# Optimization experiments

Measured on AMD Instinct MI355X. Metric: run time of the kernel, lower is better.

The kernel has to match this reference:

```python
import jax, jax.numpy as jnp
import numpy as np

INPUT_DIM, HIDDEN, LATENT, HEADS = 4, 32, 2, 4
N_NODES, N_EDGES = 50000, 800000
EPS_BN = 1e-5
NEG_SLOPE = 0.2


def _glorot(key, shape):
    fan_in, fan_out = shape[0], shape[-1]
    lim = jnp.sqrt(6.0 / (fan_in + fan_out))
    return jax.random.uniform(key, shape, jnp.float32, -lim, lim)


def setup_inputs() -> dict:
    key = jax.random.key(0)
    ks = jax.random.split(key, 20)
    x = jax.random.normal(ks[0], (N_NODES, INPUT_DIM), jnp.float32)
    edge_index = jax.random.randint(ks[1], (2, N_EDGES), 0, N_NODES, jnp.int64)

    def gat_params(k, in_ch, out_ch, heads, concat):
        k1, k2, k3 = jax.random.split(k, 3)
        W = _glorot(k1, (in_ch, heads * out_ch))
        a_src = _glorot(k2, (heads, out_ch))
        a_dst = _glorot(k3, (heads, out_ch))
        b = jnp.zeros((heads * out_ch,) if concat else (out_ch,), jnp.float32)
        return W, a_src, a_dst, b

    w_e1, as_e1, ad_e1, b_e1 = gat_params(ks[2], INPUT_DIM, HIDDEN, HEADS, True)
    w_e3, as_e3, ad_e3, b_e3 = gat_params(ks[3], HIDDEN * HEADS, LATENT, 1, False)
    w_d1, as_d1, ad_d1, b_d1 = gat_params(ks[4], LATENT, HIDDEN, HEADS, True)
    w_d3, as_d3, ad_d3, b_d3 = gat_params(ks[5], HIDDEN * HEADS, INPUT_DIM, 1, False)

    return dict(
        x=x, edge_index=edge_index,
        bn_gamma=jnp.ones((INPUT_DIM,), jnp.float32),
        bn_beta=jnp.zeros((INPUT_DIM,), jnp.float32),
        w_e1=w_e1, as_e1=as_e1, ad_e1=ad_e1, b_e1=b_e1,
        w_e3=w_e3, as_e3=as_e3, ad_e3=ad_e3, b_e3=b_e3,
        w_d1=w_d1, as_d1=as_d1, ad_d1=ad_d1, b_d1=b_d1,
        w_d3=w_d3, as_d3=as_d3, ad_d3=ad_d3, b_d3=b_d3,
    )


def gat_conv(x, src, dst, W, a_src, a_dst, b, heads, out_ch, concat):
    """PyG-style GATConv: gather -> attention -> segment softmax -> scatter."""
    n = x.shape[0]
    h = (x @ W).reshape(n, heads, out_ch)                 # [N,H,C]
    alpha_s = jnp.sum(h * a_src, axis=-1)                 # [N,H]
    alpha_d = jnp.sum(h * a_dst, axis=-1)                 # [N,H]
    e = jax.nn.leaky_relu(alpha_s[src] + alpha_d[dst], NEG_SLOPE)  # [E,H]
    # numerically-stable softmax over incoming edges of each dst node
    m = jax.ops.segment_max(e, dst, num_segments=n)
    e = jnp.exp(e - m[dst])
    s = jax.ops.segment_sum(e, dst, num_segments=n)
    a = e / (s[dst] + 1e-16)                              # [E,H]
    msg = h[src] * a[:, :, None]                          # [E,H,C]
    out = jax.ops.segment_sum(msg, dst, num_segments=n)   # [N,H,C]
    out = out.reshape(n, heads * out_ch) if concat else out.mean(axis=1)
    return out + b


def reference(x, edge_index, bn_gamma, bn_beta,
              w_e1, as_e1, ad_e1, b_e1,
              w_e3, as_e3, ad_e3, b_e3,
              w_d1, as_d1, ad_d1, b_d1,
              w_d3, as_d3, ad_d3, b_d3):
    n = x.shape[0]
    # GATConv default add_self_loops=True
    loops = jnp.arange(n, dtype=edge_index.dtype)
    src = jnp.concatenate([edge_index[0], loops])
    dst = jnp.concatenate([edge_index[1], loops])

    # BatchNorm1d (training-mode batch statistics, biased variance)
    mu = x.mean(axis=0)
    var = x.var(axis=0)
    x_in = (x - mu) * jax.lax.rsqrt(var + EPS_BN) * bn_gamma + bn_beta

    enc1 = jax.nn.relu(gat_conv(x_in, src, dst, w_e1, as_e1, ad_e1, b_e1, HEADS, HIDDEN, True))
    latent = gat_conv(enc1, src, dst, w_e3, as_e3, ad_e3, b_e3, 1, LATENT, False)
    dec1 = jax.nn.relu(gat_conv(latent, src, dst, w_d1, as_d1, ad_d1, b_d1, HEADS, HIDDEN, True))
    x_out = gat_conv(dec1, src, dst, w_d3, as_d3, ad_d3, b_d3, 1, INPUT_DIM, False)
    return x_out
```

## Files before the change

kernel.cpp:

```cpp
#include <hip/hip_runtime.h>

#define NN 50000
#define E0 800000
#define ET 850000
#define EPS_BN 1e-5f
#define SLOPE 0.2f
#define NBP 32
#define EPC 4096
#define NCH 208
#define PBITS 7
#define PSZ 128
#define NP 391
#define CAP 3072

__device__ __forceinline__ float lrelu(float v){ return v > 0.f ? v : SLOPE*v; }

__global__ __launch_bounds__(512) void k1_stage(const int* __restrict__ ei, const float* __restrict__ x,
                                                unsigned* __restrict__ pedge, int* __restrict__ gcur,
                                                float* __restrict__ part){
  __shared__ unsigned epk[EPC];
  __shared__ int cc[NP];
  __shared__ int cbase[NP];
  __shared__ float bnlds[8][8];
  const int b=blockIdx.x, t=threadIdx.x;
  for (int i=t;i<NP;i+=512) cc[i]=0;
  __syncthreads();
  int base=b*EPC;
  int nb=min(EPC, ET-base);
  for (int k=t;k<nb;k+=512){
    int e=base+k;
    int src,dst;
    if (e<E0){ src=ei[e]; dst=ei[E0+e]; } else { src=dst=e-E0; }
    epk[k]=((unsigned)src<<16)|(unsigned)dst;
    atomicAdd(&cc[dst>>PBITS],1);
  }
  __syncthreads();
  for (int i=t;i<NP;i+=512){
    int c=cc[i];
    cbase[i] = (c>0) ? atomicAdd(&gcur[i], c) : 0;
  }
  __syncthreads();
  for (int i=t;i<NP;i+=512) cc[i]=0;
  __syncthreads();
  for (int k=t;k<nb;k+=512){
    unsigned w=epk[k];
    int p=(int)((w&0xFFFFu)>>PBITS);
    int lo=atomicAdd(&cc[p],1);
    pedge[p*CAP + cbase[p] + lo]=w;
  }

  if (b<NBP){
    float s[4]={0,0,0,0}, q[4]={0,0,0,0};
    for (int n=b*512+t; n<NN; n+=NBP*512){
      float4 v = reinterpret_cast<const float4*>(x)[n];
      s[0]+=v.x; s[1]+=v.y; s[2]+=v.z; s[3]+=v.w;
      q[0]+=v.x*v.x; q[1]+=v.y*v.y; q[2]+=v.z*v.z; q[3]+=v.w*v.w;
    }
    #pragma unroll
    for (int m=1;m<64;m<<=1){
      #pragma unroll
      for (int i=0;i<4;i++){ s[i]+=__shfl_xor(s[i],m); q[i]+=__shfl_xor(q[i],m); }
    }
    int wid=t>>6, lane=t&63;
    if (lane==0){
      #pragma unroll
      for (int i=0;i<4;i++){ bnlds[wid][i]=s[i]; bnlds[wid][4+i]=q[i]; }
    }
    __syncthreads();
    if (t<8){
      float p=0.f;
      #pragma unroll
      for (int w=0;w<8;w++) p += bnlds[w][t];
      part[b*8+t]=p;
    }
  }
}

__global__ __launch_bounds__(512) void k2_fine(
    const unsigned* __restrict__ pedge, const int* __restrict__ gcur,
    int* __restrict__ rbeg, int* __restrict__ rend, unsigned short* __restrict__ ssrc,
    const float* __restrict__ part, const float* __restrict__ gamma, const float* __restrict__ beta,
    const float* __restrict__ w_e1, const float* __restrict__ as_e1, const float* __restrict__ ad_e1,
    const float* __restrict__ w_d1, const float* __restrict__ as_d1, const float* __restrict__ ad_d1,
    float* __restrict__ sclsft, float* __restrict__ fold){
  const int p=blockIdx.x, t=threadIdx.x;
  int cnt=gcur[p];
  int wbase=p*CAP;
  __shared__ int hist[PSZ], curx[PSZ];
  if (t<PSZ) hist[t]=0;
  __syncthreads();
  for (int i=t;i<cnt;i+=512) atomicAdd(&hist[pedge[wbase+i]&(PSZ-1)],1);
  __syncthreads();
  int o=(t<PSZ)?hist[t]:0;
  __syncthreads();
  int v=o;
  for (int off=1;off<PSZ;off<<=1){
    int tmp=(t>=off&&t<PSZ)?hist[t-off]:0;
    __syncthreads();
    if (t<PSZ){ v+=tmp; hist[t]=v; }
    __syncthreads();
  }
  if (t<PSZ){
    int excl=v-o;
    int d=(p<<PBITS)+t;
    if (d<NN){ rbeg[d]=wbase+excl; rend[d]=wbase+excl+o; }
    curx[t]=wbase+excl;
  }
  __syncthreads();
  for (int i=t;i<cnt;i+=512){
    unsigned w=pedge[wbase+i];
    int pos=atomicAdd(&curx[w&(PSZ-1)],1);
    ssrc[pos]=(unsigned short)(w>>16);
  }

  if (p==0){
    if (t<64){
      int ch=t&7, bslot=t>>3;
      float s=0.f;
      for (int bb=bslot; bb<NBP; bb+=8) s += part[bb*8+ch];
      s += __shfl_xor(s,8); s += __shfl_xor(s,16); s += __shfl_xor(s,32);
      float qv = __shfl(s,(t&3)+4);
      if (t<4){
        float mu  = s*(1.0f/NN);
        float var = qv*(1.0f/NN) - mu*mu;
        float scl = rsqrtf(var + EPS_BN)*gamma[t];
        sclsft[t]   = scl;
        sclsft[4+t] = beta[t] - mu*scl;
      }
    } else if (t<128){
      int u=t-64;
      if (u<32){
        int idx=u&15; int h=idx>>2; int i=idx&3;
        const float* a = (u<16) ? as_e1 : ad_e1;
        float sum=0.f;
        for (int c=0;c<32;c++) sum += w_e1[i*128+h*32+c]*a[h*32+c];
        fold[u]=sum;
      } else if (u<48){
        int idx=u-32; int j=idx&7; int h=j>>1; int i=j&1;
        const float* a = (idx<8) ? as_d1 : ad_d1;
        float sum=0.f;
        for (int c=0;c<32;c++) sum += w_d1[i*128+h*32+c]*a[h*32+c];
        fold[32+idx]=sum;
      }
    }
  }
}

__global__ __launch_bounds__(256) void eagg1(
    const float* __restrict__ x, const float* __restrict__ sclsft, const float* __restrict__ fold,
    const int* __restrict__ rbeg, const int* __restrict__ rend, const unsigned short* __restrict__ ssrc,
    const float* __restrict__ w_e1, const float* __restrict__ b_e1, const float* __restrict__ w_e3,
    float2* __restrict__ pk2){
  int dst = blockIdx.x*64 + (threadIdx.x>>2);
  int sub = threadIdx.x & 3;
  if (dst >= NN) return;
  float sc[8];
  #pragma unroll
  for (int i=0;i<8;i++) sc[i] = sclsft[i];
  float fs[16];
  #pragma unroll
  for (int i=0;i<16;i++) fs[i] = fold[i];
  float4 xd = reinterpret_cast<const float4*>(x)[dst];
  float xbd[4] = {xd.x*sc[0]+sc[4], xd.y*sc[1]+sc[5], xd.z*sc[2]+sc[6], xd.w*sc[3]+sc[7]};
  float ald[4];
  #pragma unroll
  for (int h=0;h<4;h++)
    ald[h] = xbd[0]*fold[16+h*4+0] + xbd[1]*fold[16+h*4+1]
           + xbd[2]*fold[16+h*4+2] + xbd[3]*fold[16+h*4+3];
  int r0 = rbeg[dst], r1 = rend[dst];
  float sum[4] = {0,0,0,0};
  float acc[4][4] = {{0,0,0,0},{0,0,0,0},{0,0,0,0},{0,0,0,0}};
  for (int i = r0 + sub; i < r1; i += 4){
    int s = ssrc[i];
    float4 xs = reinterpret_cast<const float4*>(x)[s];
    float xb[4] = {xs.x*sc[0]+sc[4], xs.y*sc[1]+sc[5], xs.z*sc[2]+sc[6], xs.w*sc[3]+sc[7]};
    #pragma unroll
    for (int h=0;h<4;h++){
      float a = xb[0]*fs[h*4+0] + xb[1]*fs[h*4+1] + xb[2]*fs[h*4+2] + xb[3]*fs[h*4+3];
      float w = __expf(lrelu(a + ald[h]));
      sum[h] += w;
      acc[h][0] += w*xb[0]; acc[h][1] += w*xb[1]; acc[h][2] += w*xb[2]; acc[h][3] += w*xb[3];
    }
  }
  #pragma unroll
  for (int m=1;m<4;m<<=1){
    #pragma unroll
    for (int h=0;h<4;h++){
      sum[h] += __shfl_xor(sum[h],m);
      #pragma unroll
      for (int c=0;c<4;c++) acc[h][c] += __shfl_xor(acc[h][c],m);
    }
  }
  float G0=acc[0][0], G1=acc[0][1], G2=acc[0][2], G3=acc[0][3], GS=sum[0];
  #pragma unroll
  for (int h=1;h<4;h++){
    if (sub==h){ G0=acc[h][0]; G1=acc[h][1]; G2=acc[h][2]; G3=acc[h][3]; GS=sum[h]; }
  }
  float inv = 1.f/(GS+1e-16f);
  G0*=inv; G1*=inv; G2*=inv; G3*=inv;
  float p0 = 0.f, p1 = 0.f;
  int ob = sub*32;
  #pragma unroll
  for (int q=0;q<8;q++){
    int o = ob + q*4;
    float4 b  = *reinterpret_cast<const float4*>(b_e1 + o);
    float4 w0 = *reinterpret_cast<const float4*>(w_e1 + 0*128 + o);
    float4 w1 = *reinterpret_cast<const float4*>(w_e1 + 1*128 + o);
    float4 w2 = *reinterpret_cast<const float4*>(w_e1 + 2*128 + o);
    float4 w3 = *reinterpret_cast<const float4*>(w_e1 + 3*128 + o);
    float e0 = fmaxf(b.x + G0*w0.x + G1*w1.x + G2*w2.x + G3*w3.x, 0.f);
    float e1 = fmaxf(b.y + G0*w0.y + G1*w1.y + G2*w2.y + G3*w3.y, 0.f);
    float e2 = fmaxf(b.z + G0*w0.z + G1*w1.z + G2*w2.z + G3*w3.z, 0.f);
    float e3 = fmaxf(b.w + G0*w0.w + G1*w1.w + G2*w2.w + G3*w3.w, 0.f);
    float4 wa = *reinterpret_cast<const float4*>(w_e3 + o*2);
    float4 wb = *reinterpret_cast<const float4*>(w_e3 + o*2 + 4);
    p0 += e0*wa.x + e1*wa.z + e2*wb.x + e3*wb.z;
    p1 += e0*wa.y + e1*wa.w + e2*wb.y + e3*wb.w;
  }
  p0 += __shfl_xor(p0,1); p0 += __shfl_xor(p0,2);
  p1 += __shfl_xor(p1,1); p1 += __shfl_xor(p1,2);
  if (sub==0) pk2[dst] = make_float2(p0, p1);
}

__global__ __launch_bounds__(256) void eagg2(
    const float2* __restrict__ pk2,
    const int* __restrict__ rbeg, const int* __restrict__ rend, const unsigned short* __restrict__ ssrc,
    const float* __restrict__ as_e3, const float* __restrict__ ad_e3, const float* __restrict__ b_e3,
    float2* __restrict__ lat2){
  int dst = blockIdx.x*64 + (threadIdx.x>>2);
  int sub = threadIdx.x & 3;
  if (dst >= NN) return;
  float as0 = as_e3[0], as1 = as_e3[1];
  float2 pd = pk2[dst];
  float adv = pd.x*ad_e3[0] + pd.y*ad_e3[1];
  int r0 = rbeg[dst], r1 = rend[dst];
  float sum = 0.f, a0 = 0.f, a1 = 0.f;
  for (int i = r0 + sub; i < r1; i += 4){
    int s = ssrc[i];
    float2 p = pk2[s];
    float w = __expf(lrelu(p.x*as0 + p.y*as1 + adv));
    sum += w; a0 += w*p.x; a1 += w*p.y;
  }
  #pragma unroll
  for (int m=1;m<4;m<<=1){
    sum += __shfl_xor(sum,m); a0 += __shfl_xor(a0,m); a1 += __shfl_xor(a1,m);
  }
  if (sub==0){
    float inv = 1.f/(sum+1e-16f);
    lat2[dst] = make_float2(a0*inv + b_e3[0], a1*inv + b_e3[1]);
  }
}

__global__ __launch_bounds__(256) void eagg3(
    const float2* __restrict__ lat2, const float* __restrict__ fold,
    const int* __restrict__ rbeg, const int* __restrict__ rend, const unsigned short* __restrict__ ssrc,
    const float* __restrict__ w_d1, const float* __restrict__ b_d1, const float* __restrict__ w_d3,
    float4* __restrict__ pk4){
  int dst = blockIdx.x*64 + (threadIdx.x>>2);
  int sub = threadIdx.x & 3;
  if (dst >= NN) return;
  float f3[8];
  #pragma unroll
  for (int i=0;i<8;i++) f3[i] = fold[32+i];
  float2 ld = lat2[dst];
  float ald[4];
  #pragma unroll
  for (int h=0;h<4;h++) ald[h] = ld.x*fold[40+h*2+0] + ld.y*fold[40+h*2+1];
  int r0 = rbeg[dst], r1 = rend[dst];
  float sum[4] = {0,0,0,0};
  float acc[4][2] = {{0,0},{0,0},{0,0},{0,0}};
  for (int i = r0 + sub; i < r1; i += 4){
    int s = ssrc[i];
    float2 l = lat2[s];
    #pragma unroll
    for (int h=0;h<4;h++){
      float a = l.x*f3[h*2+0] + l.y*f3[h*2+1];
      float w = __expf(lrelu(a + ald[h]));
      sum[h] += w;
      acc[h][0] += w*l.x; acc[h][1] += w*l.y;
    }
  }
  #pragma unroll
  for (int m=1;m<4;m<<=1){
    #pragma unroll
    for (int h=0;h<4;h++){
      sum[h] += __shfl_xor(sum[h],m);
      acc[h][0] += __shfl_xor(acc[h][0],m);
      acc[h][1] += __shfl_xor(acc[h][1],m);
    }
  }
  float G0=acc[0][0], G1=acc[0][1], GS=sum[0];
  #pragma unroll
  for (int h=1;h<4;h++){
    if (sub==h){ G0=acc[h][0]; G1=acc[h][1]; GS=sum[h]; }
  }
  float inv = 1.f/(GS+1e-16f);
  G0*=inv; G1*=inv;
  float p0=0.f,p1=0.f,p2=0.f,p3=0.f;
  int ob = sub*32;
  #pragma unroll
  for (int q=0;q<8;q++){
    int o = ob + q*4;
    float4 b  = *reinterpret_cast<const float4*>(b_d1 + o);
    float4 w0 = *reinterpret_cast<const float4*>(w_d1 + 0*128 + o);
    float4 w1 = *reinterpret_cast<const float4*>(w_d1 + 1*128 + o);
    float e0 = fmaxf(b.x + G0*w0.x + G1*w1.x, 0.f);
    float e1 = fmaxf(b.y + G0*w0.y + G1*w1.y, 0.f);
    float e2 = fmaxf(b.z + G0*w0.z + G1*w1.z, 0.f);
    float e3 = fmaxf(b.w + G0*w0.w + G1*w1.w, 0.f);
    float4 d0 = *reinterpret_cast<const float4*>(w_d3 + (o+0)*4);
    float4 d1 = *reinterpret_cast<const float4*>(w_d3 + (o+1)*4);
    float4 d2 = *reinterpret_cast<const float4*>(w_d3 + (o+2)*4);
    float4 d3v= *reinterpret_cast<const float4*>(w_d3 + (o+3)*4);
    p0 += e0*d0.x + e1*d1.x + e2*d2.x + e3*d3v.x;
    p1 += e0*d0.y + e1*d1.y + e2*d2.y + e3*d3v.y;
    p2 += e0*d0.z + e1*d1.z + e2*d2.z + e3*d3v.z;
    p3 += e0*d0.w + e1*d1.w + e2*d2.w + e3*d3v.w;
  }
  #pragma unroll
  for (int m=1;m<4;m<<=1){
    p0 += __shfl_xor(p0,m); p1 += __shfl_xor(p1,m);
    p2 += __shfl_xor(p2,m); p3 += __shfl_xor(p3,m);
  }
  if (sub==0) pk4[dst] = make_float4(p0,p1,p2,p3);
}

__global__ __launch_bounds__(256) void eagg4(
    const float4* __restrict__ pk4,
    const int* __restrict__ rbeg, const int* __restrict__ rend, const unsigned short* __restrict__ ssrc,
    const float* __restrict__ as_d3, const float* __restrict__ ad_d3, const float* __restrict__ b_d3,
    float* __restrict__ out){
  int dst = blockIdx.x*64 + (threadIdx.x>>2);
  int sub = threadIdx.x & 3;
  if (dst >= NN) return;
  float as0=as_d3[0], as1=as_d3[1], as2=as_d3[2], as3=as_d3[3];
  float4 hd = pk4[dst];
  float adv = hd.x*ad_d3[0] + hd.y*ad_d3[1] + hd.z*ad_d3[2] + hd.w*ad_d3[3];
  int r0 = rbeg[dst], r1 = rend[dst];
  float sum = 0.f, a0=0.f, a1=0.f, a2=0.f, a3=0.f;
  for (int i = r0 + sub; i < r1; i += 4){
    int s = ssrc[i];
    float4 f = pk4[s];
    float w = __expf(lrelu(f.x*as0 + f.y*as1 + f.z*as2 + f.w*as3 + adv));
    sum += w; a0 += w*f.x; a1 += w*f.y; a2 += w*f.z; a3 += w*f.w;
  }
  #pragma unroll
  for (int m=1;m<4;m<<=1){
    sum += __shfl_xor(sum,m);
    a0 += __shfl_xor(a0,m); a1 += __shfl_xor(a1,m);
    a2 += __shfl_xor(a2,m); a3 += __shfl_xor(a3,m);
  }
  if (sub==0){
    float inv = 1.f/(sum+1e-16f);
    reinterpret_cast<float4*>(out)[dst] =
      make_float4(a0*inv+b_d3[0], a1*inv+b_d3[1], a2*inv+b_d3[2], a3*inv+b_d3[3]);
  }
}

extern "C" void kernel_launch(void* const* d_in, const int* in_sizes, int n_in,
                              void* d_out, int out_size, void* d_ws, size_t ws_size,
                              hipStream_t stream) {
  const float* x     = (const float*)d_in[0];
  const int*   ei    = (const int*)  d_in[1];
  const float* gamma = (const float*)d_in[2];
  const float* beta  = (const float*)d_in[3];
  const float* w_e1  = (const float*)d_in[4];
  const float* as_e1 = (const float*)d_in[5];
  const float* ad_e1 = (const float*)d_in[6];
  const float* b_e1  = (const float*)d_in[7];
  const float* w_e3  = (const float*)d_in[8];
  const float* as_e3 = (const float*)d_in[9];
  const float* ad_e3 = (const float*)d_in[10];
  const float* b_e3  = (const float*)d_in[11];
  const float* w_d1  = (const float*)d_in[12];
  const float* as_d1 = (const float*)d_in[13];
  const float* ad_d1 = (const float*)d_in[14];
  const float* b_d1  = (const float*)d_in[15];
  const float* w_d3  = (const float*)d_in[16];
  const float* as_d3 = (const float*)d_in[17];
  const float* ad_d3 = (const float*)d_in[18];
  const float* b_d3  = (const float*)d_in[19];

  char* ws = (char*)d_ws;
  size_t off = 0;
  auto alloc = [&](size_t bytes)->void*{
    void* p = ws + off;
    off += (bytes + 255) & ~(size_t)255;
    return p;
  };
  unsigned* pedge   = (unsigned*)       alloc((size_t)NP*CAP*4);
  unsigned short* ssrc = (unsigned short*)alloc((size_t)NP*CAP*2);
  int*      gcur    = (int*)            alloc((size_t)NP*4);
  int*      rbeg    = (int*)            alloc((size_t)NN*4);
  int*      rend    = (int*)            alloc((size_t)NN*4);
  float*    part    = (float*)          alloc((size_t)NBP*8*4);
  float*    sclsft  = (float*)          alloc(32);
  float*    fold    = (float*)          alloc(64*4);
  float2*   pk2     = (float2*)         alloc((size_t)NN*8);
  float2*   lat2    = (float2*)         alloc((size_t)NN*8);
  float4*   pk4     = (float4*)         alloc((size_t)NN*16);

  (void)hipMemsetAsync(gcur, 0, (size_t)NP*4, stream);
  k1_stage<<<NCH, 512, 0, stream>>>(ei, x, pedge, gcur, part);
  k2_fine<<<NP, 512, 0, stream>>>(pedge, gcur, rbeg, rend, ssrc, part, gamma, beta,
                                  w_e1, as_e1, ad_e1, w_d1, as_d1, ad_d1, sclsft, fold);

  const int NAGG = (NN + 63)/64;
  eagg1<<<NAGG, 256, 0, stream>>>(x, sclsft, fold, rbeg, rend, ssrc, w_e1, b_e1, w_e3, pk2);
  eagg2<<<NAGG, 256, 0, stream>>>(pk2, rbeg, rend, ssrc, as_e3, ad_e3, b_e3, lat2);
  eagg3<<<NAGG, 256, 0, stream>>>(lat2, fold, rbeg, rend, ssrc, w_d1, b_d1, w_d3, pk4);
  eagg4<<<NAGG, 256, 0, stream>>>(pk4, rbeg, rend, ssrc, as_d3, ad_d3, b_d3, (float*)d_out);
}
```

Before: 108.0 us.

## Drop fine CSR sort; aggregate edges per partition with LDS atomics

Removes the k2_fine kernel that built a per-destination CSR (histogram, scan, scatter into ssrc). Each aggregation kernel now runs one 512-thread block per 128-destination partition. Blocks read the coarse-bucketed edges directly and accumulate softmax numerators and denominators with shared-memory float atomics. BatchNorm stats and attention folds are recomputed per block, and the per-node MLP epilogue is fused in. This saves a launch and the fine-sort pass, but every edge now costs several LDS atomics (up to 20 per edge in eagg1), and summation order becomes nondeterministic.

```diff
diff --git a/kernel.cpp b/kernel.cpp
--- a/kernel.cpp
+++ b/kernel.cpp
@@ -76,284 +76,273 @@
   }
 }
 
-__global__ __launch_bounds__(512) void k2_fine(
+__global__ __launch_bounds__(512) void eagg1(
+    const float* __restrict__ x, const float* __restrict__ part,
+    const float* __restrict__ gamma, const float* __restrict__ beta,
+    const float* __restrict__ w_e1, const float* __restrict__ as_e1, const float* __restrict__ ad_e1,
+    const float* __restrict__ b_e1, const float* __restrict__ w_e3,
     const unsigned* __restrict__ pedge, const int* __restrict__ gcur,
-    int* __restrict__ rbeg, int* __restrict__ rend, unsigned short* __restrict__ ssrc,
-    const float* __restrict__ part, const float* __restrict__ gamma, const float* __restrict__ beta,
-    const float* __restrict__ w_e1, const float* __restrict__ as_e1, const float* __restrict__ ad_e1,
-    const float* __restrict__ w_d1, const float* __restrict__ as_d1, const float* __restrict__ ad_d1,
-    float* __restrict__ sclsft, float* __restrict__ fold){
+    float2* __restrict__ pk2){
   const int p=blockIdx.x, t=threadIdx.x;
+  __shared__ float sclsft[8];
+  __shared__ float foldv[32];
+  __shared__ float adv[PSZ][4];
+  __shared__ float acc[PSZ][20];
+  if (t<64){
+    int ch=t&7, bslot=t>>3;
+    float s=0.f;
+    for (int bb=bslot; bb<NBP; bb+=8) s += part[bb*8+ch];
+    s += __shfl_xor(s,8); s += __shfl_xor(s,16); s += __shfl_xor(s,32);
+    float qv = __shfl(s,(t&3)+4);
+    if (t<4){
+      float mu  = s*(1.0f/NN);
+      float var = qv*(1.0f/NN) - mu*mu;
+      float scl = rsqrtf(var + EPS_BN)*gamma[t];
+      sclsft[t]   = scl;
+      sclsft[4+t] = beta[t] - mu*scl;
+    }
+  } else if (t<96){
+    int u=t-64;
+    int idx=u&15; int h=idx>>2; int i=idx&3;
+    const float* a=(u<16)? as_e1 : ad_e1;
+    float sum=0.f;
+    for (int c=0;c<32;c++) sum += w_e1[i*128+h*32+c]*a[h*32+c];
+    foldv[u]=sum;
+  }
+  for (int i=t;i<PSZ*20;i+=512) ((float*)acc)[i]=0.f;
+  __syncthreads();
+  int dbase=p<<PBITS;
+  if (t<PSZ){
+    int d=dbase+t;
+    if (d<NN){
+      float4 xv = reinterpret_cast<const float4*>(x)[d];
+      float xb[4]={xv.x*sclsft[0]+sclsft[4], xv.y*sclsft[1]+sclsft[5],
+                   xv.z*sclsft[2]+sclsft[6], xv.w*sclsft[3]+sclsft[7]};
+      #pragma unroll
+      for (int h=0;h<4;h++)
+        adv[t][h]=xb[0]*foldv[16+h*4+0]+xb[1]*foldv[16+h*4+1]
+                 +xb[2]*foldv[16+h*4+2]+xb[3]*foldv[16+h*4+3];
+    }
+  }
+  __syncthreads();
   int cnt=gcur[p];
   int wbase=p*CAP;
-  __shared__ int hist[PSZ], curx[PSZ];
-  if (t<PSZ) hist[t]=0;
-  __syncthreads();
-  for (int i=t;i<cnt;i+=512) atomicAdd(&hist[pedge[wbase+i]&(PSZ-1)],1);
-  __syncthreads();
-  int o=(t<PSZ)?hist[t]:0;
-  __syncthreads();
-  int v=o;
-  for (int off=1;off<PSZ;off<<=1){
-    int tmp=(t>=off&&t<PSZ)?hist[t-off]:0;
-    __syncthreads();
-    if (t<PSZ){ v+=tmp; hist[t]=v; }
-    __syncthreads();
-  }
-  if (t<PSZ){
-    int excl=v-o;
-    int d=(p<<PBITS)+t;
-    if (d<NN){ rbeg[d]=wbase+excl; rend[d]=wbase+excl+o; }
-    curx[t]=wbase+excl;
-  }
-  __syncthreads();
   for (int i=t;i<cnt;i+=512){
     unsigned w=pedge[wbase+i];
-    int pos=atomicAdd(&curx[w&(PSZ-1)],1);
-    ssrc[pos]=(unsigned short)(w>>16);
-  }
-
-  if (p==0){
-    if (t<64){
-      int ch=t&7, bslot=t>>3;
-      float s=0.f;
-      for (int bb=bslot; bb<NBP; bb+=8) s += part[bb*8+ch];
-      s += __shfl_xor(s,8); s += __shfl_xor(s,16); s += __shfl_xor(s,32);
-      float qv = __shfl(s,(t&3)+4);
-      if (t<4){
-        float mu  = s*(1.0f/NN);
-        float var = qv*(1.0f/NN) - mu*mu;
-        float scl = rsqrtf(var + EPS_BN)*gamma[t];
-        sclsft[t]   = scl;
-        sclsft[4+t] = beta[t] - mu*scl;
-      }
-    } else if (t<128){
-      int u=t-64;
-      if (u<32){
-        int idx=u&15; int h=idx>>2; int i=idx&3;
-        const float* a = (u<16) ? as_e1 : ad_e1;
-        float sum=0.f;
-        for (int c=0;c<32;c++) sum += w_e1[i*128+h*32+c]*a[h*32+c];
-        fold[u]=sum;
-      } else if (u<48){
-        int idx=u-32; int j=idx&7; int h=j>>1; int i=j&1;
-        const float* a = (idx<8) ? as_d1 : ad_d1;
-        float sum=0.f;
-        for (int c=0;c<32;c++) sum += w_d1[i*128+h*32+c]*a[h*32+c];
-        fold[32+idx]=sum;
-      }
-    }
-  }
-}
-
-__global__ __launch_bounds__(256) void eagg1(
-    const float* __restrict__ x, const float* __restrict__ sclsft, const float* __restrict__ fold,
-    const int* __restrict__ rbeg, const int* __restrict__ rend, const unsigned short* __restrict__ ssrc,
-    const float* __restrict__ w_e1, const float* __restrict__ b_e1, const float* __restrict__ w_e3,
-    float2* __restrict__ pk2){
-  int dst = blockIdx.x*64 + (threadIdx.x>>2);
-  int sub = threadIdx.x & 3;
-  if (dst >= NN) return;
-  float sc[8];
-  #pragma unroll
-  for (int i=0;i<8;i++) sc[i] = sclsft[i];
-  float fs[16];
-  #pragma unroll
-  for (int i=0;i<16;i++) fs[i] = fold[i];
-  float4 xd = reinterpret_cast<const float4*>(x)[dst];
-  float xbd[4] = {xd.x*sc[0]+sc[4], xd.y*sc[1]+sc[5], xd.z*sc[2]+sc[6], xd.w*sc[3]+sc[7]};
-  float ald[4];
-  #pragma unroll
-  for (int h=0;h<4;h++)
-    ald[h] = xbd[0]*fold[16+h*4+0] + xbd[1]*fold[16+h*4+1]
-           + xbd[2]*fold[16+h*4+2] + xbd[3]*fold[16+h*4+3];
-  int r0 = rbeg[dst], r1 = rend[dst];
-  float sum[4] = {0,0,0,0};
-  float acc[4][4] = {{0,0,0,0},{0,0,0,0},{0,0,0,0},{0,0,0,0}};
-  for (int i = r0 + sub; i < r1; i += 4){
-    int s = ssrc[i];
-    float4 xs = reinterpret_cast<const float4*>(x)[s];
-    float xb[4] = {xs.x*sc[0]+sc[4], xs.y*sc[1]+sc[5], xs.z*sc[2]+sc[6], xs.w*sc[3]+sc[7]};
+    int src=(int)(w>>16);
+    int ld=(int)(w&(PSZ-1));
+    float4 xv=reinterpret_cast<const float4*>(x)[src];
+    float xb[4]={xv.x*sclsft[0]+sclsft[4], xv.y*sclsft[1]+sclsft[5],
+                 xv.z*sclsft[2]+sclsft[6], xv.w*sclsft[3]+sclsft[7]};
     #pragma unroll
     for (int h=0;h<4;h++){
-      float a = xb[0]*fs[h*4+0] + xb[1]*fs[h*4+1] + xb[2]*fs[h*4+2] + xb[3]*fs[h*4+3];
-      float w = __expf(lrelu(a + ald[h]));
-      sum[h] += w;
-      acc[h][0] += w*xb[0]; acc[h][1] += w*xb[1]; acc[h][2] += w*xb[2]; acc[h][3] += w*xb[3];
-    }
+      float a=xb[0]*foldv[h*4+0]+xb[1]*foldv[h*4+1]
+             +xb[2]*foldv[h*4+2]+xb[3]*foldv[h*4+3]+adv[ld][h];
+      float e=__expf(lrelu(a));
+      atomicAdd(&acc[ld][h*5+0],e);
+      atomicAdd(&acc[ld][h*5+1],e*xb[0]);
+      atomicAdd(&acc[ld][h*5+2],e*xb[1]);
+      atomicAdd(&acc[ld][h*5+3],e*xb[2]);
+      atomicAdd(&acc[ld][h*5+4],e*xb[3]);
+    }
+  }
+  __syncthreads();
+  int ld=t>>2, sub=t&3;
+  int dst=dbase+ld;
+  if (dst>=NN) return;
+  float GS=acc[ld][sub*5+0];
+  float G0=acc[ld][sub*5+1], G1=acc[ld][sub*5+2], G2=acc[ld][sub*5+3], G3=acc[ld][sub*5+4];
+  float inv=1.f/(GS+1e-16f);
+  G0*=inv; G1*=inv; G2*=inv; G3*=inv;
+  float p0=0.f, p1=0.f;
+  int ob=sub*32;
+  #pragma unroll
+  for (int q=0;q<8;q++){
+    int o=ob+q*4;
+    float4 b  = *reinterpret_cast<const float4*>(b_e1+o);
+    float4 w0 = *reinterpret_cast<const float4*>(w_e1+0*128+o);
+    float4 w1 = *reinterpret_cast<const float4*>(w_e1+1*128+o);
+    float4 w2 = *reinterpret_cast<const float4*>(w_e1+2*128+o);
+    float4 w3 = *reinterpret_cast<const float4*>(w_e1+3*128+o);
+    float e0=fmaxf(b.x+G0*w0.x+G1*w1.x+G2*w2.x+G3*w3.x,0.f);
+    float e1=fmaxf(b.y+G0*w0.y+G1*w1.y+G2*w2.y+G3*w3.y,0.f);
+    float e2=fmaxf(b.z+G0*w0.z+G1*w1.z+G2*w2.z+G3*w3.z,0.f);
+    float e3=fmaxf(b.w+G0*w0.w+G1*w1.w+G2*w2.w+G3*w3.w,0.f);
+    float4 wa=*reinterpret_cast<const float4*>(w_e3+o*2);
+    float4 wb=*reinterpret_cast<const float4*>(w_e3+o*2+4);
+    p0 += e0*wa.x+e1*wa.z+e2*wb.x+e3*wb.z;
+    p1 += e0*wa.y+e1*wa.w+e2*wb.y+e3*wb.w;
+  }
+  p0+=__shfl_xor(p0,1); p0+=__shfl_xor(p0,2);
+  p1+=__shfl_xor(p1,1); p1+=__shfl_xor(p1,2);
+  if (sub==0) pk2[dst]=make_float2(p0,p1);
+}
+
+__global__ __launch_bounds__(512) void eagg2(
+    const float2* __restrict__ pk2,
+    const float* __restrict__ as_e3, const float* __restrict__ ad_e3, const float* __restrict__ b_e3,
+    const unsigned* __restrict__ pedge, const int* __restrict__ gcur,
+    float2* __restrict__ lat2){
+  const int p=blockIdx.x, t=threadIdx.x;
+  __shared__ float adv[PSZ];
+  __shared__ float acc[PSZ][3];
+  float as0=as_e3[0], as1=as_e3[1];
+  for (int i=t;i<PSZ*3;i+=512) ((float*)acc)[i]=0.f;
+  int dbase=p<<PBITS;
+  if (t<PSZ){
+    int d=dbase+t;
+    if (d<NN){
+      float2 pd=pk2[d];
+      adv[t]=pd.x*ad_e3[0]+pd.y*ad_e3[1];
+    }
+  }
+  __syncthreads();
+  int cnt=gcur[p];
+  int wbase=p*CAP;
+  for (int i=t;i<cnt;i+=512){
+    unsigned w=pedge[wbase+i];
+    int src=(int)(w>>16);
+    int ld=(int)(w&(PSZ-1));
+    float2 pv=pk2[src];
+    float e=__expf(lrelu(pv.x*as0+pv.y*as1+adv[ld]));
+    atomicAdd(&acc[ld][0],e);
+    atomicAdd(&acc[ld][1],e*pv.x);
+    atomicAdd(&acc[ld][2],e*pv.y);
+  }
+  __syncthreads();
+  if (t<PSZ){
+    int dst=dbase+t;
+    if (dst<NN){
+      float inv=1.f/(acc[t][0]+1e-16f);
+      lat2[dst]=make_float2(acc[t][1]*inv+b_e3[0], acc[t][2]*inv+b_e3[1]);
+    }
+  }
+}
+
+__global__ __launch_bounds__(512) void eagg3(
+    const float2* __restrict__ lat2,
+    const float* __restrict__ w_d1, const float* __restrict__ as_d1, const float* __restrict__ ad_d1,
+    const float* __restrict__ b_d1, const float* __restrict__ w_d3,
+    const unsigned* __restrict__ pedge, const int* __restrict__ gcur,
+    float4* __restrict__ pk4){
+  const int p=blockIdx.x, t=threadIdx.x;
+  __shared__ float fold3[16];
+  __shared__ float adv[PSZ][4];
+  __shared__ float acc[PSZ][12];
+  if (t<16){
+    int j=t&7; int h=j>>1; int i=j&1;
+    const float* a=(t<8)? as_d1 : ad_d1;
+    float sum=0.f;
+    for (int c=0;c<32;c++) sum += w_d1[i*128+h*32+c]*a[h*32+c];
+    fold3[t]=sum;
+  }
+  for (int i=t;i<PSZ*12;i+=512) ((float*)acc)[i]=0.f;
+  __syncthreads();
+  int dbase=p<<PBITS;
+  if (t<PSZ){
+    int d=dbase+t;
+    if (d<NN){
+      float2 l=lat2[d];
+      #pragma unroll
+      for (int h=0;h<4;h++) adv[t][h]=l.x*fold3[8+h*2+0]+l.y*fold3[8+h*2+1];
+    }
+  }
+  __syncthreads();
+  int cnt=gcur[p];
+  int wbase=p*CAP;
+  for (int i=t;i<cnt;i+=512){
+    unsigned w=pedge[wbase+i];
+    int src=(int)(w>>16);
+    int ld=(int)(w&(PSZ-1));
+    float2 l=lat2[src];
+    #pragma unroll
+    for (int h=0;h<4;h++){
+      float a=l.x*fold3[h*2+0]+l.y*fold3[h*2+1]+adv[ld][h];
+      float e=__expf(lrelu(a));
+      atomicAdd(&acc[ld][h*3+0],e);
+      atomicAdd(&acc[ld][h*3+1],e*l.x);
+      atomicAdd(&acc[ld][h*3+2],e*l.y);
+    }
+  }
+  __syncthreads();
+  int ld=t>>2, sub=t&3;
+  int dst=dbase+ld;
+  if (dst>=NN) return;
+  float GS=acc[ld][sub*3+0];
+  float G0=acc[ld][sub*3+1], G1=acc[ld][sub*3+2];
+  float inv=1.f/(GS+1e-16f);
+  G0*=inv; G1*=inv;
+  float p0=0.f,p1=0.f,p2=0.f,p3=0.f;
+  int ob=sub*32;
+  #pragma unroll
+  for (int q=0;q<8;q++){
+    int o=ob+q*4;
+    float4 b  = *reinterpret_cast<const float4*>(b_d1+o);
+    float4 w0 = *reinterpret_cast<const float4*>(w_d1+0*128+o);
+    float4 w1 = *reinterpret_cast<const float4*>(w_d1+1*128+o);
+    float e0=fmaxf(b.x+G0*w0.x+G1*w1.x,0.f);
+    float e1=fmaxf(b.y+G0*w0.y+G1*w1.y,0.f);
+    float e2=fmaxf(b.z+G0*w0.z+G1*w1.z,0.f);
+    float e3=fmaxf(b.w+G0*w0.w+G1*w1.w,0.f);
+    float4 d0=*reinterpret_cast<const float4*>(w_d3+(o+0)*4);
+    float4 d1=*reinterpret_cast<const float4*>(w_d3+(o+1)*4);
+    float4 d2=*reinterpret_cast<const float4*>(w_d3+(o+2)*4);
+    float4 d3v=*reinterpret_cast<const float4*>(w_d3+(o+3)*4);
+    p0+=e0*d0.x+e1*d1.x+e2*d2.x+e3*d3v.x;
+    p1+=e0*d0.y+e1*d1.y+e2*d2.y+e3*d3v.y;
+    p2+=e0*d0.z+e1*d1.z+e2*d2.z+e3*d3v.z;
+    p3+=e0*d0.w+e1*d1.w+e2*d2.w+e3*d3v.w;
   }
   #pragma unroll
   for (int m=1;m<4;m<<=1){
-    #pragma unroll
-    for (int h=0;h<4;h++){
-      sum[h] += __shfl_xor(sum[h],m);
-      #pragma unroll
-      for (int c=0;c<4;c++) acc[h][c] += __shfl_xor(acc[h][c],m);
-    }
-  }
-  float G0=acc[0][0], G1=acc[0][1], G2=acc[0][2], G3=acc[0][3], GS=sum[0];
-  #pragma unroll
-  for (int h=1;h<4;h++){
-    if (sub==h){ G0=acc[h][0]; G1=acc[h][1]; G2=acc[h][2]; G3=acc[h][3]; GS=sum[h]; }
-  }
-  float inv = 1.f/(GS+1e-16f);
-  G0*=inv; G1*=inv; G2*=inv; G3*=inv;
-  float p0 = 0.f, p1 = 0.f;
-  int ob = sub*32;
-  #pragma unroll
-  for (int q=0;q<8;q++){
-    int o = ob + q*4;
-    float4 b  = *reinterpret_cast<const float4*>(b_e1 + o);
-    float4 w0 = *reinterpret_cast<const float4*>(w_e1 + 0*128 + o);
-    float4 w1 = *reinterpret_cast<const float4*>(w_e1 + 1*128 + o);
-    float4 w2 = *reinterpret_cast<const float4*>(w_e1 + 2*128 + o);
-    float4 w3 = *reinterpret_cast<const float4*>(w_e1 + 3*128 + o);
-    float e0 = fmaxf(b.x + G0*w0.x + G1*w1.x + G2*w2.x + G3*w3.x, 0.f);
-    float e1 = fmaxf(b.y + G0*w0.y + G1*w1.y + G2*w2.y + G3*w3.y, 0.f);
-    float e2 = fmaxf(b.z + G0*w0.z + G1*w1.z + G2*w2.z + G3*w3.z, 0.f);
-    float e3 = fmaxf(b.w + G0*w0.w + G1*w1.w + G2*w2.w + G3*w3.w, 0.f);
-    float4 wa = *reinterpret_cast<const float4*>(w_e3 + o*2);
-    float4 wb = *reinterpret_cast<const float4*>(w_e3 + o*2 + 4);
-    p0 += e0*wa.x + e1*wa.z + e2*wb.x + e3*wb.z;
-    p1 += e0*wa.y + e1*wa.w + e2*wb.y + e3*wb.w;
-  }
-  p0 += __shfl_xor(p0,1); p0 += __shfl_xor(p0,2);
-  p1 += __shfl_xor(p1,1); p1 += __shfl_xor(p1,2);
-  if (sub==0) pk2[dst] = make_float2(p0, p1);
-}
-
-__global__ __launch_bounds__(256) void eagg2(
-    const float2* __restrict__ pk2,
-    const int* __restrict__ rbeg, const int* __restrict__ rend, const unsigned short* __restrict__ ssrc,
-    const float* __restrict__ as_e3, const float* __restrict__ ad_e3, const float* __restrict__ b_e3,
-    float2* __restrict__ lat2){
-  int dst = blockIdx.x*64 + (threadIdx.x>>2);
-  int sub = threadIdx.x & 3;
-  if (dst >= NN) return;
-  float as0 = as_e3[0], as1 = as_e3[1];
-  float2 pd = pk2[dst];
-  float adv = pd.x*ad_e3[0] + pd.y*ad_e3[1];
-  int r0 = rbeg[dst], r1 = rend[dst];
-  float sum = 0.f, a0 = 0.f, a1 = 0.f;
-  for (int i = r0 + sub; i < r1; i += 4){
-    int s = ssrc[i];
-    float2 p = pk2[s];
-    float w = __expf(lrelu(p.x*as0 + p.y*as1 + adv));
-    sum += w; a0 += w*p.x; a1 += w*p.y;
-  }
-  #pragma unroll
-  for (int m=1;m<4;m<<=1){
-    sum += __shfl_xor(sum,m); a0 += __shfl_xor(a0,m); a1 += __shfl_xor(a1,m);
-  }
-  if (sub==0){
-    float inv = 1.f/(sum+1e-16f);
-    lat2[dst] = make_float2(a0*inv + b_e3[0], a1*inv + b_e3[1]);
-  }
-}
-
-__global__ __launch_bounds__(256) void eagg3(
-    const float2* __restrict__ lat2, const float* __restrict__ fold,
-    const int* __restrict__ rbeg, const int* __restrict__ rend, const unsigned short* __restrict__ ssrc,
-    const float* __restrict__ w_d1, const float* __restrict__ b_d1, const float* __restrict__ w_d3,
-    float4* __restrict__ pk4){
-  int dst = blockIdx.x*64 + (threadIdx.x>>2);
-  int sub = threadIdx.x & 3;
-  if (dst >= NN) return;
-  float f3[8];
-  #pragma unroll
-  for (int i=0;i<8;i++) f3[i] = fold[32+i];
-  float2 ld = lat2[dst];
-  float ald[4];
-  #pragma unroll
-  for (int h=0;h<4;h++) ald[h] = ld.x*fold[40+h*2+0] + ld.y*fold[40+h*2+1];
-  int r0 = rbeg[dst], r1 = rend[dst];
-  float sum[4] = {0,0,0,0};
-  float acc[4][2] = {{0,0},{0,0},{0,0},{0,0}};
-  for (int i = r0 + sub; i < r1; i += 4){
-    int s = ssrc[i];
-    float2 l = lat2[s];
-    #pragma unroll
-    for (int h=0;h<4;h++){
-      float a = l.x*f3[h*2+0] + l.y*f3[h*2+1];
-      float w = __expf(lrelu(a + ald[h]));
-      sum[h] += w;
-      acc[h][0] += w*l.x; acc[h][1] += w*l.y;
-    }
-  }
-  #pragma unroll
-  for (int m=1;m<4;m<<=1){
-    #pragma unroll
-    for (int h=0;h<4;h++){
-      sum[h] += __shfl_xor(sum[h],m);
-      acc[h][0] += __shfl_xor(acc[h][0],m);
-      acc[h][1] += __shfl_xor(acc[h][1],m);
-    }
-  }
-  float G0=acc[0][0], G1=acc[0][1], GS=sum[0];
-  #pragma unroll
-  for (int h=1;h<4;h++){
-    if (sub==h){ G0=acc[h][0]; G1=acc[h][1]; GS=sum[h]; }
-  }
-  float inv = 1.f/(GS+1e-16f);
-  G0*=inv; G1*=inv;
-  float p0=0.f,p1=0.f,p2=0.f,p3=0.f;
-  int ob = sub*32;
-  #pragma unroll
-  for (int q=0;q<8;q++){
-    int o = ob + q*4;
-    float4 b  = *reinterpret_cast<const float4*>(b_d1 + o);
-    float4 w0 = *reinterpret_cast<const float4*>(w_d1 + 0*128 + o);
-    float4 w1 = *reinterpret_cast<const float4*>(w_d1 + 1*128 + o);
-    float e0 = fmaxf(b.x + G0*w0.x + G1*w1.x, 0.f);
-    float e1 = fmaxf(b.y + G0*w0.y + G1*w1.y, 0.f);
-    float e2 = fmaxf(b.z + G0*w0.z + G1*w1.z, 0.f);
-    float e3 = fmaxf(b.w + G0*w0.w + G1*w1.w, 0.f);
-    float4 d0 = *reinterpret_cast<const float4*>(w_d3 + (o+0)*4);
-    float4 d1 = *reinterpret_cast<const float4*>(w_d3 + (o+1)*4);
-    float4 d2 = *reinterpret_cast<const float4*>(w_d3 + (o+2)*4);
-    float4 d3v= *reinterpret_cast<const float4*>(w_d3 + (o+3)*4);
-    p0 += e0*d0.x + e1*d1.x + e2*d2.x + e3*d3v.x;
-    p1 += e0*d0.y + e1*d1.y + e2*d2.y + e3*d3v.y;
-    p2 += e0*d0.z + e1*d1.z + e2*d2.z + e3*d3v.z;
-    p3 += e0*d0.w + e1*d1.w + e2*d2.w + e3*d3v.w;
-  }
-  #pragma unroll
-  for (int m=1;m<4;m<<=1){
-    p0 += __shfl_xor(p0,m); p1 += __shfl_xor(p1,m);
-    p2 += __shfl_xor(p2,m); p3 += __shfl_xor(p3,m);
-  }
-  if (sub==0) pk4[dst] = make_float4(p0,p1,p2,p3);
-}
-
-__global__ __launch_bounds__(256) void eagg4(
+    p0+=__shfl_xor(p0,m); p1+=__shfl_xor(p1,m);
+    p2+=__shfl_xor(p2,m); p3+=__shfl_xor(p3,m);
+  }
+  if (sub==0) pk4[dst]=make_float4(p0,p1,p2,p3);
+}
+
+__global__ __launch_bounds__(512) void eagg4(
     const float4* __restrict__ pk4,
-    const int* __restrict__ rbeg, const int* __restrict__ rend, const unsigned short* __restrict__ ssrc,
     const float* __restrict__ as_d3, const float* __restrict__ ad_d3, const float* __restrict__ b_d3,
+    const unsigned* __restrict__ pedge, const int* __restrict__ gcur,
     float* __restrict__ out){
-  int dst = blockIdx.x*64 + (threadIdx.x>>2);
-  int sub = threadIdx.x & 3;
-  if (dst >= NN) return;
+  const int p=blockIdx.x, t=threadIdx.x;
+  __shared__ float adv[PSZ];
+  __shared__ float acc[PSZ][5];
   float as0=as_d3[0], as1=as_d3[1], as2=as_d3[2], as3=as_d3[3];
-  float4 hd = pk4[dst];
-  float adv = hd.x*ad_d3[0] + hd.y*ad_d3[1] + hd.z*ad_d3[2] + hd.w*ad_d3[3];
-  int r0 = rbeg[dst], r1 = rend[dst];
-  float sum = 0.f, a0=0.f, a1=0.f, a2=0.f, a3=0.f;
-  for (int i = r0 + sub; i < r1; i += 4){
-    int s = ssrc[i];
-    float4 f = pk4[s];
-    float w = __expf(lrelu(f.x*as0 + f.y*as1 + f.z*as2 + f.w*as3 + adv));
-    sum += w; a0 += w*f.x; a1 += w*f.y; a2 += w*f.z; a3 += w*f.w;
-  }
-  #pragma unroll
-  for (int m=1;m<4;m<<=1){
-    sum += __shfl_xor(sum,m);
-    a0 += __shfl_xor(a0,m); a1 += __shfl_xor(a1,m);
-    a2 += __shfl_xor(a2,m); a3 += __shfl_xor(a3,m);
-  }
-  if (sub==0){
-    float inv = 1.f/(sum+1e-16f);
-    reinterpret_cast<float4*>(out)[dst] =
-      make_float4(a0*inv+b_d3[0], a1*inv+b_d3[1], a2*inv+b_d3[2], a3*inv+b_d3[3]);
+  for (int i=t;i<PSZ*5;i+=512) ((float*)acc)[i]=0.f;
+  int dbase=p<<PBITS;
+  if (t<PSZ){
+    int d=dbase+t;
+    if (d<NN){
+      float4 f=pk4[d];
+      adv[t]=f.x*ad_d3[0]+f.y*ad_d3[1]+f.z*ad_d3[2]+f.w*ad_d3[3];
+    }
+  }
+  __syncthreads();
+  int cnt=gcur[p];
+  int wbase=p*CAP;
+  for (int i=t;i<cnt;i+=512){
+    unsigned w=pedge[wbase+i];
+    int src=(int)(w>>16);
+    int ld=(int)(w&(PSZ-1));
+    float4 f=pk4[src];
+    float e=__expf(lrelu(f.x*as0+f.y*as1+f.z*as2+f.w*as3+adv[ld]));
+    atomicAdd(&acc[ld][0],e);
+    atomicAdd(&acc[ld][1],e*f.x);
+    atomicAdd(&acc[ld][2],e*f.y);
+    atomicAdd(&acc[ld][3],e*f.z);
+    atomicAdd(&acc[ld][4],e*f.w);
+  }
+  __syncthreads();
+  if (t<PSZ){
+    int dst=dbase+t;
+    if (dst<NN){
+      float inv=1.f/(acc[t][0]+1e-16f);
+      reinterpret_cast<float4*>(out)[dst]=
+        make_float4(acc[t][1]*inv+b_d3[0], acc[t][2]*inv+b_d3[1],
+                    acc[t][3]*inv+b_d3[2], acc[t][4]*inv+b_d3[3]);
+    }
   }
 }
 
@@ -388,26 +377,18 @@
     off += (bytes + 255) & ~(size_t)255;
     return p;
   };
-  unsigned* pedge   = (unsigned*)       alloc((size_t)NP*CAP*4);
-  unsigned short* ssrc = (unsigned short*)alloc((size_t)NP*CAP*2);
-  int*      gcur    = (int*)            alloc((size_t)NP*4);
-  int*      rbeg    = (int*)            alloc((size_t)NN*4);
-  int*      rend    = (int*)            alloc((size_t)NN*4);
-  float*    part    = (float*)          alloc((size_t)NBP*8*4);
-  float*    sclsft  = (float*)          alloc(32);
-  float*    fold    = (float*)          alloc(64*4);
-  float2*   pk2     = (float2*)         alloc((size_t)NN*8);
-  float2*   lat2    = (float2*)         alloc((size_t)NN*8);
-  float4*   pk4     = (float4*)         alloc((size_t)NN*16);
+  unsigned* pedge  = (unsigned*)alloc((size_t)NP*CAP*4);
+  int*      gcur   = (int*)     alloc((size_t)NP*4);
+  float*    part   = (float*)   alloc((size_t)NBP*8*4);
+  float2*   pk2    = (float2*)  alloc((size_t)NN*8);
+  float2*   lat2   = (float2*)  alloc((size_t)NN*8);
+  float4*   pk4    = (float4*)  alloc((size_t)NN*16);
 
   (void)hipMemsetAsync(gcur, 0, (size_t)NP*4, stream);
   k1_stage<<<NCH, 512, 0, stream>>>(ei, x, pedge, gcur, part);
-  k2_fine<<<NP, 512, 0, stream>>>(pedge, gcur, rbeg, rend, ssrc, part, gamma, beta,
-                                  w_e1, as_e1, ad_e1, w_d1, as_d1, ad_d1, sclsft, fold);
-
-  const int NAGG = (NN + 63)/64;
-  eagg1<<<NAGG, 256, 0, stream>>>(x, sclsft, fold, rbeg, rend, ssrc, w_e1, b_e1, w_e3, pk2);
-  eagg2<<<NAGG, 256, 0, stream>>>(pk2, rbeg, rend, ssrc, as_e3, ad_e3, b_e3, lat2);
-  eagg3<<<NAGG, 256, 0, stream>>>(lat2, fold, rbeg, rend, ssrc, w_d1, b_d1, w_d3, pk4);
-  eagg4<<<NAGG, 256, 0, stream>>>(pk4, rbeg, rend, ssrc, as_d3, ad_d3, b_d3, (float*)d_out);
-}
+  eagg1<<<NP, 512, 0, stream>>>(x, part, gamma, beta, w_e1, as_e1, ad_e1, b_e1, w_e3,
+                                pedge, gcur, pk2);
+  eagg2<<<NP, 512, 0, stream>>>(pk2, as_e3, ad_e3, b_e3, pedge, gcur, lat2);
+  eagg3<<<NP, 512, 0, stream>>>(lat2, w_d1, as_d1, ad_d1, b_d1, w_d3, pedge, gcur, pk4);
+  eagg4<<<NP, 512, 0, stream>>>(pk4, as_d3, ad_d3, b_d3, pedge, gcur, (float*)d_out);
+}
```

Result: slower. 291.1 us (+169.5%).
